# Kernel optimization log

Measured on AMD Instinct MI355X. Metric: run time of the kernel, lower is better.

The kernel has to match this reference:

```python
import jax, jax.numpy as jnp
import numpy as np

# edge types from metadata: (src_type, 'to', dst_type)
NODE_SRC = [0, 1, 2, 3, 0, 1, 2, 1, 3, 1]
NODE_DST = [0, 1, 2, 3, 1, 0, 1, 2, 1, 3]
N_NODES = 30000
N_EDGES = 400000
HEADS1 = 8


def _han_conv(xs, edges, proj_W, proj_b, att_src, att_dst, k_W, k_b, q, heads):
    """Faithful port of torch_geometric HANConv (eval mode, dropout off)."""
    out_ch = proj_W.shape[-1]
    D = out_ch // heads
    N = xs[0].shape[0]
    # per-node-type projection -> [N, H, D]
    h = [(xs[t] @ proj_W[t] + proj_b[t]).reshape(N, heads, D) for t in range(4)]
    outs = {t: [] for t in range(4)}
    for e in range(10):
        s, d = NODE_SRC[e], NODE_DST[e]
        row, col = edges[e, 0], edges[e, 1]
        a_src = (h[s] * att_src[e]).sum(-1)  # [N, H]
        a_dst = (h[d] * att_dst[e]).sum(-1)  # [N, H]
        alpha = jax.nn.leaky_relu(a_src[row] + a_dst[col], 0.2)  # [E, H]
        # segment softmax over incoming edges of each dst node
        amax = jax.ops.segment_max(alpha, col, num_segments=N)
        ex = jnp.exp(alpha - amax[col])
        denom = jax.ops.segment_sum(ex, col, num_segments=N)
        w = ex / (denom[col] + 1e-16)
        msg = h[s][row] * w[:, :, None]  # [E, H, D]
        agg = jax.ops.segment_sum(msg, col, num_segments=N).reshape(N, out_ch)
        outs[d].append(jax.nn.relu(agg))
    # semantic-level attention fusion across relations ending at each node type
    res = []
    for t in range(4):
        stk = jnp.stack(outs[t])  # [M, N, C]
        score = (q * jnp.tanh(stk @ k_W + k_b).mean(axis=1)).sum(-1)  # [M]
        sattn = jax.nn.softmax(score)
        res.append((sattn[:, None, None] * stk).sum(0))  # [N, C]
    return res


def setup_inputs() -> dict:
    key = jax.random.key(0)
    ks = jax.random.split(key, 24)
    inp = {}
    for t in range(4):
        inp[f"x{t}"] = jax.random.normal(ks[t], (N_NODES, 256), dtype=jnp.float32)
    inp["edges"] = jax.random.randint(ks[4], (10, 2, N_EDGES), 0, N_NODES, dtype=jnp.int32)
    s = 0.05
    inp["proj1_W"] = jax.random.normal(ks[5], (4, 256, 128), dtype=jnp.float32) * s
    inp["proj1_b"] = jax.random.normal(ks[6], (4, 128), dtype=jnp.float32) * s
    inp["att1_src"] = jax.random.normal(ks[7], (10, 8, 16), dtype=jnp.float32) * s
    inp["att1_dst"] = jax.random.normal(ks[8], (10, 8, 16), dtype=jnp.float32) * s
    inp["k1_W"] = jax.random.normal(ks[9], (128, 128), dtype=jnp.float32) * s
    inp["k1_b"] = jax.random.normal(ks[10], (128,), dtype=jnp.float32) * s
    inp["q1"] = jax.random.normal(ks[11], (128,), dtype=jnp.float32) * s
    inp["proj2_W"] = jax.random.normal(ks[12], (4, 128, 32), dtype=jnp.float32) * s
    inp["proj2_b"] = jax.random.normal(ks[13], (4, 32), dtype=jnp.float32) * s
    inp["att2_src"] = jax.random.normal(ks[14], (10, 1, 32), dtype=jnp.float32) * s
    inp["att2_dst"] = jax.random.normal(ks[15], (10, 1, 32), dtype=jnp.float32) * s
    inp["k2_W"] = jax.random.normal(ks[16], (32, 32), dtype=jnp.float32) * s
    inp["k2_b"] = jax.random.normal(ks[17], (32,), dtype=jnp.float32) * s
    inp["q2"] = jax.random.normal(ks[18], (32,), dtype=jnp.float32) * s
    return inp


def reference(x0, x1, x2, x3, edges,
              proj1_W, proj1_b, att1_src, att1_dst, k1_W, k1_b, q1,
              proj2_W, proj2_b, att2_src, att2_dst, k2_W, k2_b, q2):
    # eval mode: all F.dropout calls are identity
    xs = [x0, x1, x2, x3]
    h = _han_conv(xs, edges, proj1_W, proj1_b, att1_src, att1_dst, k1_W, k1_b, q1, HEADS1)
    h = [jax.nn.elu(v) for v in h]
    o = _han_conv(h, edges, proj2_W, proj2_b, att2_src, att2_dst, k2_W, k2_b, q2, 1)
    # final per-node softmax over channel dim for each node type; stack since all N equal
    return jnp.stack([jax.nn.softmax(v, axis=1) for v in o])  # [4, N, 32]
```

## Files before the change

kernel.cpp:

```cpp
#include <hip/hip_runtime.h>
#include <hip/hip_fp16.h>

#define NN 30000
#define NE 400000
#define NBUCK 59
#define BPR 98
#define EPB 4096
#define CAPREG 12288
#define BCAP 12288
#define HSPLIT 15000

__constant__ int d_SRC[10] = {0,1,2,3,0,1,2,1,3,1};
__constant__ int d_DST[10] = {0,1,2,3,1,0,1,2,1,3};
__constant__ int d_RORD[10] = {1,5,7,9,0,4,2,6,3,8};
__constant__ int d_FCNT[4] = {2,4,2,2};
__constant__ int d_FREL[4][4] = {{0,5,0,0},{1,4,6,8},{2,7,0,0},{3,9,0,0}};

__constant__ int d_XRELA[8]  = {0,4,2,6,8,1,5,7};
__constant__ int d_XBASEA[8] = {0,1875,3750,5625,0,1875,3750,5625};
__constant__ int d_XCNTA[8]  = {7500,5625,3750,1875,7500,5625,3750,1875};
__constant__ int d_XRELB[8]  = {4,2,6,3,1,5,7,9};

typedef _Float16 f16x8 __attribute__((ext_vector_type(8)));
typedef float f32x4 __attribute__((ext_vector_type(4)));

struct __attribute__((aligned(8))) h2x2 { __half2 a, b; };

__global__ __launch_bounds__(256)
void proj1_k(const float* __restrict__ A0, const float* __restrict__ A1,
             const float* __restrict__ A2, const float* __restrict__ A3,
             const float* __restrict__ B, const float* __restrict__ bias,
             __half* __restrict__ C)
{
    constexpr int BM = 128, BK = 32, MR = 2, NF = 4, LDK = BK + 8;
    constexpr int K = 256, N = 128, M = NN;
    const int z = blockIdx.z;
    const float* A = (z == 0) ? A0 : (z == 1) ? A1 : (z == 2) ? A2 : A3;
    const float* Bz = B + (long)z * K * N;
    const float* bz = bias + z * N;
    __half* Cz = C + (long)z * M * N;
    const int m0 = blockIdx.x * BM;
    const int n0 = blockIdx.y * 64;
    const int tid = threadIdx.x;
    const int wv = tid >> 6;
    const int l  = tid & 63;
    const int fm = l & 15;
    const int fg = l >> 4;

    __shared__ _Float16 As[BM][LDK];
    __shared__ _Float16 Bs[64][LDK];

    f32x4 acc[MR][NF];
#pragma unroll
    for (int mr = 0; mr < MR; ++mr)
#pragma unroll
        for (int f = 0; f < NF; ++f) acc[mr][f] = (f32x4){0.f, 0.f, 0.f, 0.f};

    const int arow = tid >> 1;
    const int akc  = (tid & 1) << 4;
    const int grow = m0 + arow;

    for (int k0 = 0; k0 < K; k0 += BK) {
        f16x8 ap0, ap1;
        if (grow < M) {
            const float* aq = A + (long)grow * K + k0 + akc;
            float4 u0 = *(const float4*)aq;
            float4 u1 = *(const float4*)(aq + 4);
            float4 u2 = *(const float4*)(aq + 8);
            float4 u3 = *(const float4*)(aq + 12);
            float v[16] = {u0.x,u0.y,u0.z,u0.w, u1.x,u1.y,u1.z,u1.w,
                           u2.x,u2.y,u2.z,u2.w, u3.x,u3.y,u3.z,u3.w};
#pragma unroll
            for (int j = 0; j < 8; ++j) { ap0[j] = (_Float16)v[j]; ap1[j] = (_Float16)v[j+8]; }
        } else {
#pragma unroll
            for (int j = 0; j < 8; ++j) { ap0[j] = (_Float16)0.f; ap1[j] = (_Float16)0.f; }
        }
        *(f16x8*)&As[arow][akc]     = ap0;
        *(f16x8*)&As[arow][akc + 8] = ap1;

        {
            const int bk = tid >> 4;
            const int bn = (tid & 15) << 2;
#pragma unroll
            for (int kk = 0; kk < 2; ++kk) {
                int kr = bk + kk * 16;
                float4 u = *(const float4*)(Bz + (long)(k0 + kr) * N + n0 + bn);
                Bs[bn + 0][kr] = (_Float16)u.x;
                Bs[bn + 1][kr] = (_Float16)u.y;
                Bs[bn + 2][kr] = (_Float16)u.z;
                Bs[bn + 3][kr] = (_Float16)u.w;
            }
        }
        __syncthreads();

        f16x8 a0 = *(const f16x8*)&As[wv * 32 + fm][fg * 8];
        f16x8 a1 = *(const f16x8*)&As[wv * 32 + 16 + fm][fg * 8];
#pragma unroll
        for (int f = 0; f < NF; ++f) {
            f16x8 b = *(const f16x8*)&Bs[f * 16 + fm][fg * 8];
            acc[0][f] = __builtin_amdgcn_mfma_f32_16x16x32_f16(a0, b, acc[0][f], 0, 0, 0);
            acc[1][f] = __builtin_amdgcn_mfma_f32_16x16x32_f16(a1, b, acc[1][f], 0, 0, 0);
        }
        __syncthreads();
    }

#pragma unroll
    for (int f = 0; f < NF; ++f) {
        float bzv = bz[n0 + f * 16 + fm];
#pragma unroll
        for (int mr = 0; mr < MR; ++mr)
#pragma unroll
            for (int i = 0; i < 4; ++i) {
                int gr = m0 + wv * 32 + mr * 16 + fg * 4 + i;
                if (gr < M) Cz[(long)gr * N + n0 + f * 16 + fm] = __float2half(acc[mr][f][i] + bzv);
            }
    }
}

template<int BN>
__global__ __launch_bounds__(256)
void mgemm_k(const _Float16* __restrict__ Ah, long sA,
             const float* __restrict__ B, long sB,
             const float* __restrict__ bias, long sBias,
             float* __restrict__ C, long sC,
             int M, int K, int N, int relu_a, int epi)
{
    constexpr int BM = 128, BK = 32, MR = 2;
    constexpr int NF = BN / 16;
    constexpr int LDK = BK + 8;
    const int z = blockIdx.z;
    Ah += (long)z * sA;
    B += (long)z * sB;
    bias += (long)z * sBias;
    C += (long)z * sC;
    const int m0 = blockIdx.x * BM;
    const int n0 = blockIdx.y * BN;
    const int tid = threadIdx.x;
    const int wv = tid >> 6;
    const int l  = tid & 63;
    const int fm = l & 15;
    const int fg = l >> 4;

    __shared__ _Float16 As[BM][LDK];
    __shared__ _Float16 Bs[BN][LDK];
    __shared__ float red[4][BN];

    f32x4 acc[MR][NF];
#pragma unroll
    for (int mr = 0; mr < MR; ++mr)
#pragma unroll
        for (int f = 0; f < NF; ++f) acc[mr][f] = (f32x4){0.f, 0.f, 0.f, 0.f};

    const int arow = tid >> 1;
    const int akc  = (tid & 1) << 4;
    const int grow = m0 + arow;

    for (int k0 = 0; k0 < K; k0 += BK) {
        f16x8 ap0, ap1;
        if (grow < M) {
            const _Float16* aq = Ah + (long)grow * K + k0 + akc;
            ap0 = *(const f16x8*)aq;
            ap1 = *(const f16x8*)(aq + 8);
            if (relu_a) {
#pragma unroll
                for (int j = 0; j < 8; ++j) {
                    ap0[j] = ap0[j] > (_Float16)0.f ? ap0[j] : (_Float16)0.f;
                    ap1[j] = ap1[j] > (_Float16)0.f ? ap1[j] : (_Float16)0.f;
                }
            }
        } else {
#pragma unroll
            for (int j = 0; j < 8; ++j) { ap0[j] = (_Float16)0.f; ap1[j] = (_Float16)0.f; }
        }
        *(f16x8*)&As[arow][akc]     = ap0;
        *(f16x8*)&As[arow][akc + 8] = ap1;

        if constexpr (BN == 64) {
            const int bk = tid >> 4;
            const int bn = (tid & 15) << 2;
#pragma unroll
            for (int kk = 0; kk < 2; ++kk) {
                int kr = bk + kk * 16;
                float4 u = *(const float4*)(B + (long)(k0 + kr) * N + n0 + bn);
                Bs[bn + 0][kr] = (_Float16)u.x;
                Bs[bn + 1][kr] = (_Float16)u.y;
                Bs[bn + 2][kr] = (_Float16)u.z;
                Bs[bn + 3][kr] = (_Float16)u.w;
            }
        } else {
            const int bk = tid >> 3;
            const int bn = (tid & 7) << 2;
            float4 u = *(const float4*)(B + (long)(k0 + bk) * N + n0 + bn);
            Bs[bn + 0][bk] = (_Float16)u.x;
            Bs[bn + 1][bk] = (_Float16)u.y;
            Bs[bn + 2][bk] = (_Float16)u.z;
            Bs[bn + 3][bk] = (_Float16)u.w;
        }
        __syncthreads();

        f16x8 a0 = *(const f16x8*)&As[wv * 32 + fm][fg * 8];
        f16x8 a1 = *(const f16x8*)&As[wv * 32 + 16 + fm][fg * 8];
#pragma unroll
        for (int f = 0; f < NF; ++f) {
            f16x8 b = *(const f16x8*)&Bs[f * 16 + fm][fg * 8];
            acc[0][f] = __builtin_amdgcn_mfma_f32_16x16x32_f16(a0, b, acc[0][f], 0, 0, 0);
            acc[1][f] = __builtin_amdgcn_mfma_f32_16x16x32_f16(a1, b, acc[1][f], 0, 0, 0);
        }
        __syncthreads();
    }

    if (epi == 2) {
        __half* Ch = (__half*)C;
#pragma unroll
        for (int f = 0; f < NF; ++f) {
            float bz = bias[n0 + f * 16 + fm];
#pragma unroll
            for (int mr = 0; mr < MR; ++mr)
#pragma unroll
                for (int i = 0; i < 4; ++i) {
                    int gr = m0 + wv * 32 + mr * 16 + fg * 4 + i;
                    if (gr < M) Ch[(long)gr * N + n0 + f * 16 + fm] = __float2half(acc[mr][f][i] + bz);
                }
        }
    } else {
#pragma unroll
        for (int f = 0; f < NF; ++f) {
            float bz = bias[n0 + f * 16 + fm];
            float s = 0.f;
#pragma unroll
            for (int mr = 0; mr < MR; ++mr)
#pragma unroll
                for (int i = 0; i < 4; ++i) {
                    int gr = m0 + wv * 32 + mr * 16 + fg * 4 + i;
                    if (gr < M) s += tanhf(acc[mr][f][i] + bz);
                }
            s += __shfl_xor(s, 16, 64);
            s += __shfl_xor(s, 32, 64);
            if (fg == 0) red[wv][f * 16 + fm] = s;
        }
        __syncthreads();
        if (tid < BN) {
            float s = red[0][tid] + red[1][tid] + red[2][tid] + red[3][tid];
            unsafeAtomicAdd(&C[n0 + tid], s);
        }
    }
}

__global__ __launch_bounds__(256)
void init_k(int* __restrict__ binCur, float* __restrict__ colsum)
{
    int i = blockIdx.x * 256 + threadIdx.x;
    if (i < 10 * NBUCK) binCur[i] = (i % NBUCK) * CAPREG;
    if (i < 1632) colsum[i] = 0.f;
}

__global__ __launch_bounds__(256)
void csr_binA(const int* __restrict__ edges, int* __restrict__ binCur,
              unsigned* __restrict__ binned)
{
    __shared__ int lcnt[NBUCK];
    __shared__ int gbase[NBUCK];
    int rel = blockIdx.x / BPR;
    int blk = blockIdx.x - rel * BPR;
    int base = blk * EPB;
    int tid = threadIdx.x;
    for (int b = tid; b < NBUCK; b += 256) lcnt[b] = 0;
    __syncthreads();
    const int* er = edges + (long)rel * 2 * NE;
    const int* ec = er + NE;
    unsigned pk[16];
    unsigned mt[16];
#pragma unroll
    for (int k = 0; k < 16; ++k) {
        int i = base + k * 256 + tid;
        if (i < NE) {
            int r = er[i];
            int c = ec[i];
            int b = c >> 9;
            int lo = atomicAdd(&lcnt[b], 1);
            pk[k] = ((unsigned)c << 15) | (unsigned)r;
            mt[k] = ((unsigned)b << 16) | (unsigned)lo;
        } else {
            mt[k] = 0xFFFFFFFFu;
        }
    }
    __syncthreads();
    if (tid < NBUCK) gbase[tid] = atomicAdd(&binCur[rel * NBUCK + tid], lcnt[tid]);
    __syncthreads();
    unsigned* bn = binned + (long)rel * NBUCK * CAPREG;
#pragma unroll
    for (int k = 0; k < 16; ++k) {
        if (mt[k] != 0xFFFFFFFFu) {
            int b = mt[k] >> 16;
            int lo = mt[k] & 0xFFFF;
            bn[gbase[b] + lo] = pk[k];
        }
    }
}

__global__ __launch_bounds__(256)
void csr_binB(const int* __restrict__ binCur, const unsigned* __restrict__ binned,
              int* __restrict__ off_all, unsigned short* __restrict__ rows,
              int* __restrict__ splits)
{
    __shared__ int cntS[512];
    __shared__ int cntL[512];
    __shared__ int lcur[512];
    __shared__ int hcur[512];
    __shared__ int part[256];
    __shared__ int buf[BCAP];
    int rel = blockIdx.x / NBUCK;
    int bkt = blockIdx.x - rel * NBUCK;
    const unsigned* bn = binned + ((long)rel * NBUCK + bkt) * CAPREG;
    int* off = off_all + rel * (NN + 1);
    int* spl = splits + rel * NN;
    unsigned short* rw = rows + (long)rel * NE;
    int cnt = binCur[rel * NBUCK + bkt] - bkt * CAPREG;
    int gbase = 0;
    for (int b = 0; b < bkt; ++b) gbase += binCur[rel * NBUCK + b] - b * CAPREG;
    int nb0 = bkt << 9;
    int nb1 = min(nb0 + 512, NN);
    int nloc = nb1 - nb0;
    int tid = threadIdx.x;
    if (bkt == 0 && tid == 0) off[NN] = NE;

    cntS[tid] = 0; cntS[tid + 256] = 0;
    cntL[tid] = 0; cntL[tid + 256] = 0;
    __syncthreads();
    for (int j = tid; j < cnt; j += 256) {
        unsigned p = bn[j];
        int c = (int)(p >> 15);
        int r = (int)(p & 0x7FFF);
        atomicAdd(&cntS[c - nb0], 1);
        if (r < HSPLIT) atomicAdd(&cntL[c - nb0], 1);
    }
    __syncthreads();
    int c0 = cntS[2 * tid], c1 = cntS[2 * tid + 1];
    part[tid] = c0 + c1;
    __syncthreads();
    for (int d = 1; d < 256; d <<= 1) {
        int u = (tid >= d) ? part[tid - d] : 0;
        __syncthreads();
        part[tid] += u;
        __syncthreads();
    }
    int pre = (tid == 0) ? 0 : part[tid - 1];
    cntS[2 * tid] = pre;
    cntS[2 * tid + 1] = pre + c0;
    __syncthreads();
    for (int i = tid; i < nloc; i += 256) {
        off[nb0 + i] = gbase + cntS[i];
        spl[nb0 + i] = gbase + cntS[i] + cntL[i];
    }
    lcur[tid] = cntS[tid];               lcur[tid + 256] = cntS[tid + 256];
    hcur[tid] = cntS[tid] + cntL[tid];   hcur[tid + 256] = cntS[tid + 256] + cntL[tid + 256];
    __syncthreads();
    if (cnt <= BCAP) {
        for (int j = tid; j < cnt; j += 256) {
            unsigned p = bn[j];
            int r = (int)(p & 0x7FFF);
            int c = (int)(p >> 15);
            int pos = (r < HSPLIT) ? atomicAdd(&lcur[c - nb0], 1)
                                   : atomicAdd(&hcur[c - nb0], 1);
            buf[pos] = r;
        }
        __syncthreads();
        for (int i = tid; i < cnt; i += 256) rw[gbase + i] = (unsigned short)buf[i];
    } else {
        for (int j = tid; j < cnt; j += 256) {
            unsigned p = bn[j];
            int r = (int)(p & 0x7FFF);
            int c = (int)(p >> 15);
            int pos = (r < HSPLIT) ? atomicAdd(&lcur[c - nb0], 1)
                                   : atomicAdd(&hcur[c - nb0], 1);
            rw[gbase + pos] = (unsigned short)r;
        }
    }
}

__global__ __launch_bounds__(256)
void attn_dots1(const __half* __restrict__ h1h,
                const float* __restrict__ att_src,
                const float* __restrict__ att_dst,
                float* __restrict__ asrc, float* __restrict__ adst)
{
    int gid = blockIdx.x * 256 + threadIdx.x;
    int wave = gid >> 6;
    int lane = gid & 63;
    if (wave >= 4 * NN) return;
    int t = wave / NN;
    int n = wave - t * NN;
    __half2 hh = *(const __half2*)&h1h[(long)(t * NN + n) * 128 + 2 * lane];
    float2 hv = __half22float2(hh);
    const int SRCc[10] = {0,1,2,3,0,1,2,1,3,1};
    const int DSTc[10] = {0,1,2,3,1,0,1,2,1,3};
#pragma unroll
    for (int e = 0; e < 10; ++e) {
        if (SRCc[e] == t) {
            float2 av = *(const float2*)&att_src[e * 128 + 2 * lane];
            float p = hv.x * av.x + hv.y * av.y;
#pragma unroll
            for (int off = 1; off < 8; off <<= 1) p += __shfl_xor(p, off, 64);
            if ((lane & 7) == 0) asrc[(long)(e * NN + n) * 8 + (lane >> 3)] = p;
        }
        if (DSTc[e] == t) {
            float2 bv = *(const float2*)&att_dst[e * 128 + 2 * lane];
            float p = hv.x * bv.x + hv.y * bv.y;
#pragma unroll
            for (int off = 1; off < 8; off <<= 1) p += __shfl_xor(p, off, 64);
            if ((lane & 7) == 0) adst[(long)(e * NN + n) * 8 + (lane >> 3)] = p;
        }
    }
}

__global__ __launch_bounds__(256)
void gather_agg1_all(const int* __restrict__ csr_off, const int* __restrict__ splits,
                     const unsigned short* __restrict__ csr_rows,
                     const float* __restrict__ asrc1, const float* __restrict__ adst1,
                     const __half* __restrict__ h1h, __half* __restrict__ slots16)
{
    int g = blockIdx.x;
    int xcd = g & 7;
    int slot = g >> 3;
    int e, i;
    if (slot < d_XCNTA[xcd]) { e = d_XRELA[xcd]; i = d_XBASEA[xcd] + slot; }
    else                     { e = d_XRELB[xcd]; i = slot - d_XCNTA[xcd]; }
    int node = i * 4 + (threadIdx.x >> 6);
    int lane = threadIdx.x & 63;
    if (node >= NN) return;
    const int* off = csr_off + e * (NN + 1);
    const int* spl = splits + e * NN;
    const unsigned short* rows = csr_rows + (long)e * NE;
    const float* asrc_e = asrc1 + (long)e * NN * 8;
    const float* adst_e = adst1 + (long)e * NN * 8;
    const _Float16* h1s = (const _Float16*)h1h + (long)d_SRC[e] * NN * 128;
    __half* out = slots16 + (long)e * NN * 128;

    const int g2  = lane >> 4;
    const int s16 = lane & 15;
    const int hv  = s16 >> 1;
    const int eA  = lane >> 3;
    const int hA  = lane & 7;
    int beg = off[node], end = off[node + 1];
    int mid = spl[node];
    float adA = adst_e[node * 8 + hA];
    float den = (g2 == 0) ? 1e-16f : 0.f;
    float a0 = 0.f, a1 = 0.f, a2 = 0.f, a3 = 0.f;
    float a4 = 0.f, a5 = 0.f, a6 = 0.f, a7 = 0.f;

#define GA1_STEP(i)                                                              \
    {                                                                            \
        int e0 = 4 * (i) + g2;                                                   \
        float wi = __shfl(w, e0 * 8 + hv, 64);                                   \
        int ri = __shfl(r, e0 * 8, 64);                                          \
        f16x8 v = *(const f16x8*)(h1s + (long)ri * 128 + 8 * s16);               \
        den += wi;                                                               \
        a0 += wi * (float)v[0]; a1 += wi * (float)v[1];                          \
        a2 += wi * (float)v[2]; a3 += wi * (float)v[3];                          \
        a4 += wi * (float)v[4]; a5 += wi * (float)v[5];                          \
        a6 += wi * (float)v[6]; a7 += wi * (float)v[7];                          \
    }

#pragma unroll 1
    for (int seg = 0; seg < 2; ++seg) {
        int s0 = seg ? mid : beg;
        int s1 = seg ? end : mid;
        for (int j0 = s0; j0 < s1; j0 += 8) {
            int jj = j0 + eA;
            bool ok = jj < s1;
            int r = (int)rows[ok ? jj : s0];
            float aw = asrc_e[r * 8 + hA] + adA;
            float al = aw > 0.f ? aw : 0.2f * aw;
            float w = ok ? __expf(al) : 0.f;
            int cnt = s1 - j0;
            GA1_STEP(0)
            if (cnt > 4) { GA1_STEP(1) }
        }
    }
#undef GA1_STEP
#pragma unroll
    for (int m = 16; m < 64; m <<= 1) {
        a0 += __shfl_xor(a0, m, 64); a1 += __shfl_xor(a1, m, 64);
        a2 += __shfl_xor(a2, m, 64); a3 += __shfl_xor(a3, m, 64);
        a4 += __shfl_xor(a4, m, 64); a5 += __shfl_xor(a5, m, 64);
        a6 += __shfl_xor(a6, m, 64); a7 += __shfl_xor(a7, m, 64);
        den += __shfl_xor(den, m, 64);
    }
    if (g2 == 0) {
        float inv = 1.0f / den;
        f16x8 o;
        o[0] = (_Float16)(a0 * inv); o[1] = (_Float16)(a1 * inv);
        o[2] = (_Float16)(a2 * inv); o[3] = (_Float16)(a3 * inv);
        o[4] = (_Float16)(a4 * inv); o[5] = (_Float16)(a5 * inv);
        o[6] = (_Float16)(a6 * inv); o[7] = (_Float16)(a7 * inv);
        *(f16x8*)((_Float16*)out + (long)node * 128 + 8 * s16) = o;
    }
}

__global__ __launch_bounds__(256)
void fusion_all(const __half* __restrict__ slots16, const float* __restrict__ sattn,
                __half* __restrict__ h1f)
{
    int t = blockIdx.y;
    int idx = blockIdx.x * 256 + threadIdx.x;
    if (idx >= NN * 32) return;
    int c4 = idx & 31;
    int n = idx >> 5;
    long off = (long)n * 128 + c4 * 4;
    int cnt = d_FCNT[t];
    float o0 = 0.f, o1 = 0.f, o2 = 0.f, o3 = 0.f;
    for (int j = 0; j < cnt; ++j) {
        int e = d_FREL[t][j];
        float w = sattn[e];
        const __half* p = slots16 + (long)e * NN * 128 + off;
        float2 v01 = __half22float2(*(const __half2*)p);
        float2 v23 = __half22float2(*(const __half2*)(p + 2));
        o0 += w * fmaxf(v01.x, 0.f);
        o1 += w * fmaxf(v01.y, 0.f);
        o2 += w * fmaxf(v23.x, 0.f);
        o3 += w * fmaxf(v23.y, 0.f);
    }
    o0 = o0 > 0.f ? o0 : __expf(o0) - 1.f;
    o1 = o1 > 0.f ? o1 : __expf(o1) - 1.f;
    o2 = o2 > 0.f ? o2 : __expf(o2) - 1.f;
    o3 = o3 > 0.f ? o3 : __expf(o3) - 1.f;
    __half* q = h1f + (long)t * NN * 128 + off;
    *(__half2*)q = __floats2half2_rn(o0, o1);
    *(__half2*)(q + 2) = __floats2half2_rn(o2, o3);
}

__global__ __launch_bounds__(256)
void attn_dots2(const __half* __restrict__ h2h,
                const float* __restrict__ att_src,
                const float* __restrict__ att_dst,
                float* __restrict__ asrc, float* __restrict__ adst)
{
    int gid = blockIdx.x * 256 + threadIdx.x;
    int p = gid >> 5;
    int l = gid & 31;
    if (p >= 10 * NN) return;
    int e = p / NN, n = p - e * NN;
    int s = d_SRC[e], d = d_DST[e];
    float hs = __half2float(h2h[(long)(s * NN + n) * 32 + l]);
    float hd = __half2float(h2h[(long)(d * NN + n) * 32 + l]);
    float ps = hs * att_src[e * 32 + l];
    float pd = hd * att_dst[e * 32 + l];
#pragma unroll
    for (int off = 1; off < 32; off <<= 1) {
        ps += __shfl_xor(ps, off, 64);
        pd += __shfl_xor(pd, off, 64);
    }
    if (l == 0) { asrc[e * NN + n] = ps; adst[e * NN + n] = pd; }
}

__global__ __launch_bounds__(256)
void gather_agg2(const int* __restrict__ csr_off,
                 const unsigned short* __restrict__ csr_rows,
                 const __half* __restrict__ h2h,
                 const float* __restrict__ asrc, const float* __restrict__ adst,
                 __half* __restrict__ agg2h)
{
    int e = d_RORD[blockIdx.y];
    int node = blockIdx.x * 8 + (threadIdx.x >> 5);
    int lane = threadIdx.x & 31;
    if (node >= NN) return;
    const int* off = csr_off + e * (NN + 1);
    const unsigned short* rows = csr_rows + (long)e * NE;
    const __half* h2s = h2h + (long)d_SRC[e] * NN * 32;
    const float* as = asrc + e * NN;
    const int slot = lane >> 3;
    const int sub = lane & 7;
    float ad = adst[e * NN + node];
    int beg = off[node], end = off[node + 1];
    float den = (slot == 0) ? 1e-16f : 0.f;
    float a0 = 0.f, a1 = 0.f, a2 = 0.f, a3 = 0.f;

#define GA2_STEP(i)                                                              \
    {                                                                            \
        int e0 = (i) * 4 + slot;                                                 \
        float wi = __shfl(w, e0, 32);                                            \
        int ri = __shfl(r, e0, 32);                                              \
        h2x2 v = *(const h2x2*)(h2s + (long)ri * 32 + 4 * sub);                  \
        float2 f0 = __half22float2(v.a);                                         \
        float2 f1 = __half22float2(v.b);                                         \
        den += wi;                                                               \
        a0 += wi * f0.x; a1 += wi * f0.y; a2 += wi * f1.x; a3 += wi * f1.y;      \
    }

    for (int j0 = beg; j0 < end; j0 += 32) {
        int jj = j0 + lane;
        bool ok = jj < end;
        int r = (int)rows[ok ? jj : beg];
        float a = as[r] + ad;
        a = a > 0.f ? a : 0.2f * a;
        float w = ok ? __expf(a) : 0.f;
        int cnt = end - j0;
        if (cnt >= 32) {
            GA2_STEP(0) GA2_STEP(1) GA2_STEP(2) GA2_STEP(3)
            GA2_STEP(4) GA2_STEP(5) GA2_STEP(6) GA2_STEP(7)
        } else {
            int it = (cnt + 3) >> 2;
            for (int i = 0; i < it; ++i) GA2_STEP(i)
        }
    }
#undef GA2_STEP
#pragma unroll
    for (int m = 8; m < 32; m <<= 1) {
        a0 += __shfl_xor(a0, m, 32);
        a1 += __shfl_xor(a1, m, 32);
        a2 += __shfl_xor(a2, m, 32);
        a3 += __shfl_xor(a3, m, 32);
        den += __shfl_xor(den, m, 32);
    }
    if (slot == 0) {
        float inv = 1.0f / den;
        h2x2 o;
        o.a = __floats2half2_rn(a0 * inv, a1 * inv);
        o.b = __floats2half2_rn(a2 * inv, a3 * inv);
        *(h2x2*)(agg2h + ((long)e * NN + node) * 32 + 4 * sub) = o;
    }
}

__global__ void score_all_k(const float* __restrict__ colsum, const float* __restrict__ q,
                            float* __restrict__ sattn, int C)
{
    __shared__ float sc[10];
    int tid = threadIdx.x;
    if (tid < 10) {
        float s = 0.f;
        for (int c = 0; c < C; ++c) s += q[c] * colsum[tid * C + c];
        sc[tid] = s / (float)NN;
    }
    __syncthreads();
    if (tid < 4) {
        float mx = -1e30f;
        for (int m = 0; m < 10; ++m) if (d_DST[m] == tid) mx = fmaxf(mx, sc[m]);
        float ex[10];
        float sum = 0.f;
        for (int m = 0; m < 10; ++m) {
            ex[m] = 0.f;
            if (d_DST[m] == tid) { ex[m] = __expf(sc[m] - mx); sum += ex[m]; }
        }
        for (int m = 0; m < 10; ++m) if (d_DST[m] == tid) sattn[m] = ex[m] / sum;
    }
}

__global__ __launch_bounds__(256)
void final_softmax(const __half* __restrict__ agg, const float* __restrict__ sattn,
                   float* __restrict__ out)
{
    int gid = blockIdx.x * 256 + threadIdx.x;
    int c = gid & 31;
    int p = gid >> 5;
    if (p >= 4 * NN) return;
    int t = p / NN, n = p - t * NN;
    float f = 0.f;
    for (int m = 0; m < 10; ++m) {
        if (d_DST[m] != t) continue;
        f += sattn[m] * fmaxf(__half2float(agg[(long)(m * NN + n) * 32 + c]), 0.f);
    }
    float mx = f;
#pragma unroll
    for (int off = 1; off < 32; off <<= 1) mx = fmaxf(mx, __shfl_xor(mx, off, 64));
    float ex = __expf(f - mx);
    float sm = ex;
#pragma unroll
    for (int off = 1; off < 32; off <<= 1) sm += __shfl_xor(sm, off, 64);
    out[(long)(t * NN + n) * 32 + c] = ex / sm;
}

extern "C" void kernel_launch(void* const* d_in, const int* in_sizes, int n_in,
                              void* d_out, int out_size, void* d_ws, size_t ws_size,
                              hipStream_t stream) {
    const float* x[4] = {
        (const float*)d_in[0], (const float*)d_in[1],
        (const float*)d_in[2], (const float*)d_in[3]};
    const int* edges = (const int*)d_in[4];
    const float* W1    = (const float*)d_in[5];
    const float* b1    = (const float*)d_in[6];
    const float* att1s = (const float*)d_in[7];
    const float* att1d = (const float*)d_in[8];
    const float* k1W   = (const float*)d_in[9];
    const float* k1b   = (const float*)d_in[10];
    const float* q1    = (const float*)d_in[11];
    const float* W2    = (const float*)d_in[12];
    const float* b2    = (const float*)d_in[13];
    const float* att2s = (const float*)d_in[14];
    const float* att2d = (const float*)d_in[15];
    const float* k2W   = (const float*)d_in[16];
    const float* k2b   = (const float*)d_in[17];
    const float* q2    = (const float*)d_in[18];

    float* W = (float*)d_ws;
    __half* h1h    = (__half*)W;
    __half* h1f    = (__half*)W;
    __half* h2h    = (__half*)(W + 7680000);
    __half* slots16 = (__half*)(W + 15360000);
    __half* agg2h  = (__half*)(W + 15360000);
    unsigned* binned = (unsigned*)(W + 15360000);
    int*   binCur  = (int*)(W + 15360000 + 7249920);
    float* asrc1   = W + 34560000;
    float* adst1   = W + 36960000;
    float* asrc2   = W + 36960000;
    float* adst2   = W + 37260000;
    float* colsum1 = W + 39360000;
    float* sattn1  = W + 39361280;
    float* colsum2 = W + 39361296;
    float* sattn2  = W + 39361616;
    int*   csr_off = (int*)(W + 39361640);
    unsigned short* csr_row = (unsigned short*)(csr_off + 300016);
    int*   csr_spl = (int*)(csr_row + 4000000);

    init_k<<<7, 256, 0, stream>>>(binCur, colsum1);
    csr_binA<<<BPR * 10, 256, 0, stream>>>(edges, binCur, binned);
    csr_binB<<<NBUCK * 10, 256, 0, stream>>>(binCur, binned, csr_off, csr_row, csr_spl);

    proj1_k<<<dim3(235, 2, 4), 256, 0, stream>>>(
        x[0], x[1], x[2], x[3], W1, b1, h1h);

    attn_dots1<<<30000, 256, 0, stream>>>(h1h, att1s, att1d, asrc1, adst1);

    gather_agg1_all<<<75000, 256, 0, stream>>>(
        csr_off, csr_spl, csr_row, asrc1, adst1, h1h, slots16);

    mgemm_k<64><<<dim3(235, 2, 10), 256, 0, stream>>>(
        (const _Float16*)slots16, (long)NN * 128, k1W, 0, k1b, 0,
        colsum1, 128, NN, 128, 128, 1, 1);
    score_all_k<<<1, 64, 0, stream>>>(colsum1, q1, sattn1, 128);

    fusion_all<<<dim3(3750, 4), 256, 0, stream>>>(slots16, sattn1, h1f);

    mgemm_k<32><<<dim3(235, 1, 4), 256, 0, stream>>>(
        (const _Float16*)h1f, (long)NN * 128, W2, 128L * 32, b2, 32,
        (float*)h2h, (long)NN * 16, NN, 128, 32, 0, 2);

    attn_dots2<<<37500, 256, 0, stream>>>(h2h, att2s, att2d, asrc2, adst2);
    gather_agg2<<<dim3(3750, 10), 256, 0, stream>>>(
        csr_off, csr_row, h2h, asrc2, adst2, agg2h);

    mgemm_k<32><<<dim3(235, 1, 10), 256, 0, stream>>>(
        (const _Float16*)agg2h, (long)NN * 32, k2W, 0, k2b, 0,
        colsum2, 32L, NN, 32, 32, 1, 1);
    score_all_k<<<1, 64, 0, stream>>>(colsum2, q2, sattn2, 32);
    final_softmax<<<15000, 256, 0, stream>>>(agg2h, sattn2, (float*)d_out);
}
```

Baseline: 728.5 us.

## Widen GEMM N-tiles to 128, drop CSR row split, prefetch gather loads

Proj1 and the k1 GEMM now compute the full 128-column width in one block instead of two 64-wide blocks. This halves A-tile loads and launches but doubles accumulator registers per thread. The CSR build no longer splits each node's edges into low and high source-row halves, which removes the split array and its extra shared-memory atomics. The layer-1 gather loop now software-prefetches the next group's row index and source attention score, trading the locality of the old split ordering for overlapped load latency.

```diff
diff --git a/kernel.cpp b/kernel.cpp
--- a/kernel.cpp
+++ b/kernel.cpp
@@ -8,7 +8,6 @@
 #define EPB 4096
 #define CAPREG 12288
 #define BCAP 12288
-#define HSPLIT 15000
 
 __constant__ int d_SRC[10] = {0,1,2,3,0,1,2,1,3,1};
 __constant__ int d_DST[10] = {0,1,2,3,1,0,1,2,1,3};
@@ -32,7 +31,7 @@
              const float* __restrict__ B, const float* __restrict__ bias,
              __half* __restrict__ C)
 {
-    constexpr int BM = 128, BK = 32, MR = 2, NF = 4, LDK = BK + 8;
+    constexpr int BM = 128, BK = 32, MR = 2, NF = 8, LDK = BK + 8;
     constexpr int K = 256, N = 128, M = NN;
     const int z = blockIdx.z;
     const float* A = (z == 0) ? A0 : (z == 1) ? A1 : (z == 2) ? A2 : A3;
@@ -40,7 +39,6 @@
     const float* bz = bias + z * N;
     __half* Cz = C + (long)z * M * N;
     const int m0 = blockIdx.x * BM;
-    const int n0 = blockIdx.y * 64;
     const int tid = threadIdx.x;
     const int wv = tid >> 6;
     const int l  = tid & 63;
@@ -48,7 +46,7 @@
     const int fg = l >> 4;
 
     __shared__ _Float16 As[BM][LDK];
-    __shared__ _Float16 Bs[64][LDK];
+    __shared__ _Float16 Bs[128][LDK];
 
     f32x4 acc[MR][NF];
 #pragma unroll
@@ -81,15 +79,21 @@
 
         {
             const int bk = tid >> 4;
-            const int bn = (tid & 15) << 2;
+            const int bn = (tid & 15) << 3;
 #pragma unroll
             for (int kk = 0; kk < 2; ++kk) {
                 int kr = bk + kk * 16;
-                float4 u = *(const float4*)(Bz + (long)(k0 + kr) * N + n0 + bn);
-                Bs[bn + 0][kr] = (_Float16)u.x;
-                Bs[bn + 1][kr] = (_Float16)u.y;
-                Bs[bn + 2][kr] = (_Float16)u.z;
-                Bs[bn + 3][kr] = (_Float16)u.w;
+                const float* bp = Bz + (long)(k0 + kr) * N + bn;
+                float4 u0 = *(const float4*)bp;
+                float4 u1 = *(const float4*)(bp + 4);
+                Bs[bn + 0][kr] = (_Float16)u0.x;
+                Bs[bn + 1][kr] = (_Float16)u0.y;
+                Bs[bn + 2][kr] = (_Float16)u0.z;
+                Bs[bn + 3][kr] = (_Float16)u0.w;
+                Bs[bn + 4][kr] = (_Float16)u1.x;
+                Bs[bn + 5][kr] = (_Float16)u1.y;
+                Bs[bn + 6][kr] = (_Float16)u1.z;
+                Bs[bn + 7][kr] = (_Float16)u1.w;
             }
         }
         __syncthreads();
@@ -107,13 +111,13 @@
 
 #pragma unroll
     for (int f = 0; f < NF; ++f) {
-        float bzv = bz[n0 + f * 16 + fm];
+        float bzv = bz[f * 16 + fm];
 #pragma unroll
         for (int mr = 0; mr < MR; ++mr)
 #pragma unroll
             for (int i = 0; i < 4; ++i) {
                 int gr = m0 + wv * 32 + mr * 16 + fg * 4 + i;
-                if (gr < M) Cz[(long)gr * N + n0 + f * 16 + fm] = __float2half(acc[mr][f][i] + bzv);
+                if (gr < M) Cz[(long)gr * N + f * 16 + fm] = __float2half(acc[mr][f][i] + bzv);
             }
     }
 }
@@ -176,17 +180,23 @@
         *(f16x8*)&As[arow][akc]     = ap0;
         *(f16x8*)&As[arow][akc + 8] = ap1;
 
-        if constexpr (BN == 64) {
+        if constexpr (BN == 128) {
             const int bk = tid >> 4;
-            const int bn = (tid & 15) << 2;
+            const int bn = (tid & 15) << 3;
 #pragma unroll
             for (int kk = 0; kk < 2; ++kk) {
                 int kr = bk + kk * 16;
-                float4 u = *(const float4*)(B + (long)(k0 + kr) * N + n0 + bn);
-                Bs[bn + 0][kr] = (_Float16)u.x;
-                Bs[bn + 1][kr] = (_Float16)u.y;
-                Bs[bn + 2][kr] = (_Float16)u.z;
-                Bs[bn + 3][kr] = (_Float16)u.w;
+                const float* bp = B + (long)(k0 + kr) * N + n0 + bn;
+                float4 u0 = *(const float4*)bp;
+                float4 u1 = *(const float4*)(bp + 4);
+                Bs[bn + 0][kr] = (_Float16)u0.x;
+                Bs[bn + 1][kr] = (_Float16)u0.y;
+                Bs[bn + 2][kr] = (_Float16)u0.z;
+                Bs[bn + 3][kr] = (_Float16)u0.w;
+                Bs[bn + 4][kr] = (_Float16)u1.x;
+                Bs[bn + 5][kr] = (_Float16)u1.y;
+                Bs[bn + 6][kr] = (_Float16)u1.z;
+                Bs[bn + 7][kr] = (_Float16)u1.w;
             }
         } else {
             const int bk = tid >> 3;
@@ -301,20 +311,16 @@
 
 __global__ __launch_bounds__(256)
 void csr_binB(const int* __restrict__ binCur, const unsigned* __restrict__ binned,
-              int* __restrict__ off_all, unsigned short* __restrict__ rows,
-              int* __restrict__ splits)
+              int* __restrict__ off_all, unsigned short* __restrict__ rows)
 {
     __shared__ int cntS[512];
-    __shared__ int cntL[512];
     __shared__ int lcur[512];
-    __shared__ int hcur[512];
     __shared__ int part[256];
     __shared__ int buf[BCAP];
     int rel = blockIdx.x / NBUCK;
     int bkt = blockIdx.x - rel * NBUCK;
     const unsigned* bn = binned + ((long)rel * NBUCK + bkt) * CAPREG;
     int* off = off_all + rel * (NN + 1);
-    int* spl = splits + rel * NN;
     unsigned short* rw = rows + (long)rel * NE;
     int cnt = binCur[rel * NBUCK + bkt] - bkt * CAPREG;
     int gbase = 0;
@@ -326,14 +332,10 @@
     if (bkt == 0 && tid == 0) off[NN] = NE;
 
     cntS[tid] = 0; cntS[tid + 256] = 0;
-    cntL[tid] = 0; cntL[tid + 256] = 0;
     __syncthreads();
     for (int j = tid; j < cnt; j += 256) {
-        unsigned p = bn[j];
-        int c = (int)(p >> 15);
-        int r = (int)(p & 0x7FFF);
+        int c = (int)(bn[j] >> 15);
         atomicAdd(&cntS[c - nb0], 1);
-        if (r < HSPLIT) atomicAdd(&cntL[c - nb0], 1);
     }
     __syncthreads();
     int c0 = cntS[2 * tid], c1 = cntS[2 * tid + 1];
@@ -349,20 +351,15 @@
     cntS[2 * tid] = pre;
     cntS[2 * tid + 1] = pre + c0;
     __syncthreads();
-    for (int i = tid; i < nloc; i += 256) {
-        off[nb0 + i] = gbase + cntS[i];
-        spl[nb0 + i] = gbase + cntS[i] + cntL[i];
-    }
-    lcur[tid] = cntS[tid];               lcur[tid + 256] = cntS[tid + 256];
-    hcur[tid] = cntS[tid] + cntL[tid];   hcur[tid + 256] = cntS[tid + 256] + cntL[tid + 256];
+    for (int i = tid; i < nloc; i += 256) off[nb0 + i] = gbase + cntS[i];
+    lcur[tid] = cntS[tid]; lcur[tid + 256] = cntS[tid + 256];
     __syncthreads();
     if (cnt <= BCAP) {
         for (int j = tid; j < cnt; j += 256) {
             unsigned p = bn[j];
             int r = (int)(p & 0x7FFF);
             int c = (int)(p >> 15);
-            int pos = (r < HSPLIT) ? atomicAdd(&lcur[c - nb0], 1)
-                                   : atomicAdd(&hcur[c - nb0], 1);
+            int pos = atomicAdd(&lcur[c - nb0], 1);
             buf[pos] = r;
         }
         __syncthreads();
@@ -372,8 +369,7 @@
             unsigned p = bn[j];
             int r = (int)(p & 0x7FFF);
             int c = (int)(p >> 15);
-            int pos = (r < HSPLIT) ? atomicAdd(&lcur[c - nb0], 1)
-                                   : atomicAdd(&hcur[c - nb0], 1);
+            int pos = atomicAdd(&lcur[c - nb0], 1);
             rw[gbase + pos] = (unsigned short)r;
         }
     }
@@ -415,7 +411,7 @@
 }
 
 __global__ __launch_bounds__(256)
-void gather_agg1_all(const int* __restrict__ csr_off, const int* __restrict__ splits,
+void gather_agg1_all(const int* __restrict__ csr_off,
                      const unsigned short* __restrict__ csr_rows,
                      const float* __restrict__ asrc1, const float* __restrict__ adst1,
                      const __half* __restrict__ h1h, __half* __restrict__ slots16)
@@ -430,7 +426,6 @@
     int lane = threadIdx.x & 63;
     if (node >= NN) return;
     const int* off = csr_off + e * (NN + 1);
-    const int* spl = splits + e * NN;
     const unsigned short* rows = csr_rows + (long)e * NE;
     const float* asrc_e = asrc1 + (long)e * NN * 8;
     const float* adst_e = adst1 + (long)e * NN * 8;
@@ -443,7 +438,6 @@
     const int eA  = lane >> 3;
     const int hA  = lane & 7;
     int beg = off[node], end = off[node + 1];
-    int mid = spl[node];
     float adA = adst_e[node * 8 + hA];
     float den = (g2 == 0) ? 1e-16f : 0.f;
     float a0 = 0.f, a1 = 0.f, a2 = 0.f, a3 = 0.f;
@@ -462,20 +456,28 @@
         a6 += wi * (float)v[6]; a7 += wi * (float)v[7];                          \
     }
 
-#pragma unroll 1
-    for (int seg = 0; seg < 2; ++seg) {
-        int s0 = seg ? mid : beg;
-        int s1 = seg ? end : mid;
-        for (int j0 = s0; j0 < s1; j0 += 8) {
-            int jj = j0 + eA;
-            bool ok = jj < s1;
-            int r = (int)rows[ok ? jj : s0];
-            float aw = asrc_e[r * 8 + hA] + adA;
+    if (beg < end) {
+        int j0 = beg;
+        int jj = j0 + eA;
+        bool ok = jj < end;
+        int r = (int)rows[ok ? jj : beg];
+        float aw = asrc_e[r * 8 + hA] + adA;
+        while (true) {
             float al = aw > 0.f ? aw : 0.2f * aw;
             float w = ok ? __expf(al) : 0.f;
-            int cnt = s1 - j0;
+            int j1 = j0 + 8;
+            int rn = r; float awn = 0.f; bool okn = false;
+            if (j1 < end) {
+                int jn = j1 + eA;
+                okn = jn < end;
+                rn = (int)rows[okn ? jn : beg];
+                awn = asrc_e[rn * 8 + hA] + adA;
+            }
+            int cnt = end - j0;
             GA1_STEP(0)
             if (cnt > 4) { GA1_STEP(1) }
+            if (j1 >= end) break;
+            j0 = j1; r = rn; aw = awn; ok = okn;
         }
     }
 #undef GA1_STEP
@@ -710,21 +712,20 @@
     float* sattn2  = W + 39361616;
     int*   csr_off = (int*)(W + 39361640);
     unsigned short* csr_row = (unsigned short*)(csr_off + 300016);
-    int*   csr_spl = (int*)(csr_row + 4000000);
 
     init_k<<<7, 256, 0, stream>>>(binCur, colsum1);
     csr_binA<<<BPR * 10, 256, 0, stream>>>(edges, binCur, binned);
-    csr_binB<<<NBUCK * 10, 256, 0, stream>>>(binCur, binned, csr_off, csr_row, csr_spl);
-
-    proj1_k<<<dim3(235, 2, 4), 256, 0, stream>>>(
+    csr_binB<<<NBUCK * 10, 256, 0, stream>>>(binCur, binned, csr_off, csr_row);
+
+    proj1_k<<<dim3(235, 1, 4), 256, 0, stream>>>(
         x[0], x[1], x[2], x[3], W1, b1, h1h);
 
     attn_dots1<<<30000, 256, 0, stream>>>(h1h, att1s, att1d, asrc1, adst1);
 
     gather_agg1_all<<<75000, 256, 0, stream>>>(
-        csr_off, csr_spl, csr_row, asrc1, adst1, h1h, slots16);
-
-    mgemm_k<64><<<dim3(235, 2, 10), 256, 0, stream>>>(
+        csr_off, csr_row, asrc1, adst1, h1h, slots16);
+
+    mgemm_k<128><<<dim3(235, 1, 10), 256, 0, stream>>>(
         (const _Float16*)slots16, (long)NN * 128, k1W, 0, k1b, 0,
         colsum1, 128, NN, 128, 128, 1, 1);
     score_all_k<<<1, 64, 0, stream>>>(colsum1, q1, sattn1, 128);
```

New measurement: 752.8 us. +3.3%, slower.
